# Performance work log

Measured on AMD Instinct MI355X. Metric: run time of the kernel, lower is better.

## Reference

```python
import jax, jax.numpy as jnp
import numpy as np

NUM_USERS = 100000
NUM_ITEMS = 50000
DIM_H = 64
NUM_LAYERS = 4
NUM_EDGES = 2000000


def setup_inputs() -> dict:
    key = jax.random.key(0)
    k1, k2, k3, k4 = jax.random.split(key, 4)
    emb_users = jax.random.normal(k1, (NUM_USERS, DIM_H), dtype=jnp.float32) * 0.01
    emb_items = jax.random.normal(k2, (NUM_ITEMS, DIM_H), dtype=jnp.float32) * 0.01
    edge_users = jax.random.randint(k3, (NUM_EDGES,), 0, NUM_USERS, dtype=jnp.int64)
    edge_items = jax.random.randint(k4, (NUM_EDGES,), 0, NUM_ITEMS, dtype=jnp.int64)
    edge_values = jnp.ones((NUM_EDGES,), dtype=jnp.float32)
    return {"emb_users": emb_users, "emb_items": emb_items,
            "edge_users": edge_users, "edge_items": edge_items,
            "edge_values": edge_values}


def reference(emb_users, emb_items, edge_users, edge_items, edge_values):
    U = emb_users.shape[0]
    I = emb_items.shape[0]
    N = U + I
    # Symmetric bipartite adjacency in COO form: (u, i+U) and (i+U, u).
    rows = jnp.concatenate([edge_users, edge_items + U])
    cols = jnp.concatenate([edge_items + U, edge_users])
    vals = jnp.concatenate([edge_values, edge_values])
    # D^{-1/2} A D^{-1/2} normalization (inf -> 0 for isolated nodes).
    deg = jax.ops.segment_sum(vals, rows, num_segments=N)
    dinv = jnp.where(deg > 0, jax.lax.rsqrt(jnp.maximum(deg, 1e-12)), 0.0)
    nvals = dinv[rows] * vals * dinv[cols]

    emb = jnp.concatenate([emb_users, emb_items])  # [N, d]
    acc = emb  # running sum over layer outputs (incl. layer 0)
    e = emb
    for _ in range(NUM_LAYERS):
        # SpMM: e <- A_norm @ e via gather + segment-sum scatter
        e = jax.ops.segment_sum(nvals[:, None] * e[cols], rows, num_segments=N)
        acc = acc + e
    alpha = 1.0 / (NUM_LAYERS + 1)
    # Original computes alpha * mean(stack(embs)), i.e. sum / (L+1)^2.
    emb_final = alpha * (acc / (NUM_LAYERS + 1))
    embf_users = emb_final[:U]
    embf_items = emb_final[U:]
    return (embf_users, emb_users, embf_items, emb_items)
```

## Files before the change

kernel.cpp:

```cpp
#include <hip/hip_runtime.h>


static inline size_t align_up(size_t x, size_t a) { return (x + a - 1) & ~(a - 1); }

#define BS_LOG 10
#define NBA 160
#define KB  1024
#define ENT 4096

__device__ inline unsigned short f32_to_bf16(float f) {
    unsigned int u = __float_as_uint(f);
    unsigned int r = (u + 0x7FFFu + ((u >> 16) & 1u)) >> 16;
    return (unsigned short)r;
}
__device__ inline float bf16_to_f32(unsigned short h) {
    return __uint_as_float(((unsigned int)h) << 16);
}
__device__ inline float bf16_lo(unsigned int d) {
    return __uint_as_float(d << 16);
}
__device__ inline float bf16_hi(unsigned int d) {
    return __uint_as_float(d & 0xFFFF0000u);
}

__global__ __launch_bounds__(256) void k_bucket_count(
        const int* __restrict__ eu, const int* __restrict__ ei,
        int* __restrict__ bh, int U, int E, int NB, int CH) {
    __shared__ int hist[NBA];
    int k = blockIdx.x;
    int t = threadIdx.x;
    if (t < NBA) hist[t] = 0;
    __syncthreads();
    int lo = k * CH, hi = min(E, lo + CH);
    for (int i = lo + t; i < hi; i += 256) {
        int u  = eu[i];
        int it = ei[i] + U;
        atomicAdd(&hist[u >> BS_LOG], 1);
        atomicAdd(&hist[it >> BS_LOG], 1);
    }
    __syncthreads();
    if (t < NB) bh[k * NBA + t] = hist[t];
}

__global__ __launch_bounds__(256) void k_scan_blocks(
        int* __restrict__ bh, int* __restrict__ total, int NB) {
    __shared__ int s[256];
    int b = blockIdx.x;
    int t = threadIdx.x;
    int k0 = t * 4;
    int vals[4];
    int sum = 0;
    #pragma unroll
    for (int j = 0; j < 4; ++j) { vals[j] = bh[(k0 + j) * NBA + b]; sum += vals[j]; }
    s[t] = sum;
    __syncthreads();
    for (int d = 1; d < 256; d <<= 1) {
        int v = (t >= d) ? s[t - d] : 0;
        __syncthreads();
        s[t] += v;
        __syncthreads();
    }
    int run = s[t] - sum;
    #pragma unroll
    for (int j = 0; j < 4; ++j) { int v = vals[j]; bh[(k0 + j) * NBA + b] = run; run += v; }
    if (t == 255) total[b] = run;
}

__global__ __launch_bounds__(256) void k_scan_buckets(
        const int* __restrict__ total, int* __restrict__ bbase, int NB) {
    __shared__ int s[256];
    int t = threadIdx.x;
    int v = (t < NB) ? (((total[t] + 3) & ~3) + 3072) : 0;
    s[t] = v;
    __syncthreads();
    for (int d = 1; d < 256; d <<= 1) {
        int x = (t >= d) ? s[t - d] : 0;
        __syncthreads();
        s[t] += x;
        __syncthreads();
    }
    if (t < NB) bbase[t] = s[t] - v;
}

__global__ __launch_bounds__(256) void k_bucket_scatter(
        const int* __restrict__ eu, const int* __restrict__ ei,
        const float* __restrict__ ev, const int* __restrict__ bh,
        int2* __restrict__ gb, int U, int E, int NB, int CH, int CAP) {
    __shared__ uint2 sent[ENT];
    __shared__ int   sdst[ENT];
    __shared__ int   lcur[NBA];
    __shared__ int   ldif[NBA];
    __shared__ int   sscan[256];
    __shared__ int   stot;
    int k = blockIdx.x;
    int t = threadIdx.x;
    if (t < NBA) lcur[t] = 0;
    __syncthreads();
    int lo = k * CH, hi = min(E, lo + CH);
    for (int i = lo + t; i < hi; i += 256) {
        int u  = eu[i];
        int it = ei[i] + U;
        atomicAdd(&lcur[u >> BS_LOG], 1);
        atomicAdd(&lcur[it >> BS_LOG], 1);
    }
    __syncthreads();
    int c = (t < NB) ? lcur[t] : 0;
    sscan[t] = c;
    __syncthreads();
    for (int d = 1; d < 256; d <<= 1) {
        int v = (t >= d) ? sscan[t - d] : 0;
        __syncthreads();
        sscan[t] += v;
        __syncthreads();
    }
    if (t < NB) {
        int st = sscan[t] - c;
        lcur[t] = st;
        ldif[t] = t * CAP + bh[k * NBA + t] - st;
    }
    if (t == 255) stot = sscan[255];
    __syncthreads();
    for (int i = lo + t; i < hi; i += 256) {
        int u  = eu[i];
        int it = ei[i] + U;
        unsigned vb = __float_as_uint(ev[i]);
        int b1 = u >> BS_LOG;
        int s1 = atomicAdd(&lcur[b1], 1);
        sent[s1] = make_uint2((unsigned)((u & 1023) | (it << 10)), vb);
        sdst[s1] = ldif[b1] + s1;
        int b2 = it >> BS_LOG;
        int s2 = atomicAdd(&lcur[b2], 1);
        sent[s2] = make_uint2((unsigned)((it & 1023) | (u << 10)), vb);
        sdst[s2] = ldif[b2] + s2;
    }
    __syncthreads();
    int tot = stot;
    for (int i = t; i < tot; i += 256) {
        uint2 e = sent[i];
        gb[sdst[i]] = make_int2((int)e.x, (int)e.y);
    }
}

__global__ __launch_bounds__(1024) void k_bucket_csr(
        const int2* __restrict__ gb, const int* __restrict__ total,
        const int* __restrict__ bbase,
        int* __restrict__ offs, int* __restrict__ cnt,
        float* __restrict__ dinv, float* __restrict__ dsq,
        int2* __restrict__ csr, int N, int CAP) {
    __shared__ int   hist[1024];
    __shared__ float degf[1024];
    __shared__ int   offl[1024];
    __shared__ int   scan[1024];
    int b = blockIdx.x;
    int t = threadIdx.x;
    int n0 = b << BS_LOG;
    int nbc = min(1024, N - n0);
    int cb = min(total[b], CAP);
    int base = bbase[b];
    const int2* gbb = gb + (size_t)b * CAP;

    hist[t] = 0;
    degf[t] = 0.f;
    __syncthreads();
    for (int i = t; i < cb; i += 1024) {
        int2 e = gbb[i];
        int rl = e.x & 1023;
        atomicAdd(&hist[rl], 1);
        atomicAdd(&degf[rl], __int_as_float(e.y));
    }
    __syncthreads();
    int h = hist[t];
    int h4 = (h + 3) & ~3;
    scan[t] = h4;
    __syncthreads();
    for (int d = 1; d < 1024; d <<= 1) {
        int v = (t >= d) ? scan[t - d] : 0;
        __syncthreads();
        scan[t] += v;
        __syncthreads();
    }
    int off4 = scan[t] - h4;
    offl[t] = off4;
    if (t < nbc) {
        int node = n0 + t;
        offs[node] = base + off4;
        cnt[node]  = h;
        float s = degf[t];
        bool pos = (s > 0.0f);
        dinv[node] = pos ? rsqrtf(fmaxf(s, 1e-12f)) : 0.0f;
        dsq[node]  = pos ? sqrtf(s) : 0.0f;
        for (int p = h; p < h4; ++p)
            csr[base + off4 + p] = make_int2(0, 0);
    }
    hist[t] = 0;
    __syncthreads();
    for (int i = t; i < cb; i += 1024) {
        int2 e = gbb[i];
        int rl = e.x & 1023;
        int col = (int)(((unsigned)e.x) >> 10);
        int tk = atomicAdd(&hist[rl], 1);
        csr[base + offl[rl] + tk] = make_int2(col, e.y);
    }
}

__global__ void k_init(const float4* __restrict__ emb_u, const float4* __restrict__ emb_i,
                       const float* __restrict__ dinv,
                       ushort4* __restrict__ g0, int U16, int N16) {
    int i = blockIdx.x * blockDim.x + threadIdx.x;
    if (i >= N16) return;
    float4 v = (i < U16) ? emb_u[i] : emb_i[i - U16];
    float d = dinv[i >> 4];
    ushort4 o;
    o.x = f32_to_bf16(v.x * d);
    o.y = f32_to_bf16(v.y * d);
    o.z = f32_to_bf16(v.z * d);
    o.w = f32_to_bf16(v.w * d);
    g0[i] = o;
}

__global__ __launch_bounds__(256) void k_layer(
        const uint4* __restrict__ gin, uint4* __restrict__ gout,
        const float* __restrict__ dinv,
        const int* __restrict__ offs, const int* __restrict__ cnt,
        const int2* __restrict__ csr, int N) {
    int gtid = blockIdx.x * blockDim.x + threadIdx.x;
    int row = gtid >> 3;
    unsigned q = threadIdx.x & 7;
    if (row >= N) return;
    int base = offs[row];
    int c = cnt[row];
    int nIter = (c + 3) >> 2;

    float a0 = 0.f, a1 = 0.f, a2 = 0.f, a3 = 0.f;
    float a4 = 0.f, a5 = 0.f, a6 = 0.f, a7 = 0.f;

    const uint4* ep4 = (const uint4*)(csr + base);
    uint4 E0 = make_uint4(0, 0, 0, 0), E1 = E0;
    if (nIter > 0) { E0 = ep4[0]; E1 = ep4[1]; }

    for (int i = 0; i < nIter; ++i) {
        uint4 G0 = gin[(E0.x << 3) | q];
        uint4 G1 = gin[(E0.z << 3) | q];
        uint4 G2 = gin[(E1.x << 3) | q];
        uint4 G3 = gin[(E1.z << 3) | q];
        uint4 P0 = ep4[2 * i + 2];
        uint4 P1 = ep4[2 * i + 3];
        float w0 = __uint_as_float(E0.y);
        float w1 = __uint_as_float(E0.w);
        float w2 = __uint_as_float(E1.y);
        float w3 = __uint_as_float(E1.w);
        a0 += w0 * bf16_lo(G0.x); a1 += w0 * bf16_hi(G0.x);
        a2 += w0 * bf16_lo(G0.y); a3 += w0 * bf16_hi(G0.y);
        a4 += w0 * bf16_lo(G0.z); a5 += w0 * bf16_hi(G0.z);
        a6 += w0 * bf16_lo(G0.w); a7 += w0 * bf16_hi(G0.w);
        a0 += w1 * bf16_lo(G1.x); a1 += w1 * bf16_hi(G1.x);
        a2 += w1 * bf16_lo(G1.y); a3 += w1 * bf16_hi(G1.y);
        a4 += w1 * bf16_lo(G1.z); a5 += w1 * bf16_hi(G1.z);
        a6 += w1 * bf16_lo(G1.w); a7 += w1 * bf16_hi(G1.w);
        a0 += w2 * bf16_lo(G2.x); a1 += w2 * bf16_hi(G2.x);
        a2 += w2 * bf16_lo(G2.y); a3 += w2 * bf16_hi(G2.y);
        a4 += w2 * bf16_lo(G2.z); a5 += w2 * bf16_hi(G2.z);
        a6 += w2 * bf16_lo(G2.w); a7 += w2 * bf16_hi(G2.w);
        a0 += w3 * bf16_lo(G3.x); a1 += w3 * bf16_hi(G3.x);
        a2 += w3 * bf16_lo(G3.y); a3 += w3 * bf16_hi(G3.y);
        a4 += w3 * bf16_lo(G3.z); a5 += w3 * bf16_hi(G3.z);
        a6 += w3 * bf16_lo(G3.w); a7 += w3 * bf16_hi(G3.w);
        E0 = P0; E1 = P1;
    }

    float dr = dinv[row];
    float d2 = dr * dr;
    uint4 o;
    o.x = (unsigned int)f32_to_bf16(d2 * a0) | ((unsigned int)f32_to_bf16(d2 * a1) << 16);
    o.y = (unsigned int)f32_to_bf16(d2 * a2) | ((unsigned int)f32_to_bf16(d2 * a3) << 16);
    o.z = (unsigned int)f32_to_bf16(d2 * a4) | ((unsigned int)f32_to_bf16(d2 * a5) << 16);
    o.w = (unsigned int)f32_to_bf16(d2 * a6) | ((unsigned int)f32_to_bf16(d2 * a7) << 16);
    gout[((unsigned)row << 3) | q] = o;
}

__global__ void k_final(const float4* __restrict__ emb_u, const float4* __restrict__ emb_i,
                        const ushort4* __restrict__ g1, const ushort4* __restrict__ g2,
                        const ushort4* __restrict__ g3, const ushort4* __restrict__ g4,
                        const float* __restrict__ dsq,
                        float4* __restrict__ out, int U16, int I16) {
    int i = blockIdx.x * blockDim.x + threadIdx.x;
    int total = 2 * U16 + 2 * I16;
    if (i >= total) return;
    const float s = 1.0f / 25.0f;
    float4 r;
    if (i < U16 || (i >= 2 * U16 && i < 2 * U16 + I16)) {
        int gi, node;
        float4 e0;
        if (i < U16) { gi = i; node = i >> 4; e0 = emb_u[i]; }
        else { int j = i - 2 * U16; gi = U16 + j; node = (U16 >> 4) + (j >> 4); e0 = emb_i[j]; }
        float d = dsq[node];
        ushort4 a = g1[gi], b = g2[gi], cc = g3[gi], dd = g4[gi];
        float gx = bf16_to_f32(a.x) + bf16_to_f32(b.x) + bf16_to_f32(cc.x) + bf16_to_f32(dd.x);
        float gy = bf16_to_f32(a.y) + bf16_to_f32(b.y) + bf16_to_f32(cc.y) + bf16_to_f32(dd.y);
        float gz = bf16_to_f32(a.z) + bf16_to_f32(b.z) + bf16_to_f32(cc.z) + bf16_to_f32(dd.z);
        float gw = bf16_to_f32(a.w) + bf16_to_f32(b.w) + bf16_to_f32(cc.w) + bf16_to_f32(dd.w);
        r = make_float4((e0.x + d * gx) * s, (e0.y + d * gy) * s,
                        (e0.z + d * gz) * s, (e0.w + d * gw) * s);
    } else if (i < 2 * U16) {
        r = emb_u[i - U16];
    } else {
        r = emb_i[i - 2 * U16 - I16];
    }
    out[i] = r;
}

extern "C" void kernel_launch(void* const* d_in, const int* in_sizes, int n_in,
                              void* d_out, int out_size, void* d_ws, size_t ws_size,
                              hipStream_t stream) {
    const float* emb_u = (const float*)d_in[0];
    const float* emb_i = (const float*)d_in[1];
    const int*   eu    = (const int*)d_in[2];
    const int*   ei    = (const int*)d_in[3];
    const float* ev    = (const float*)d_in[4];

    const int U = in_sizes[0] / 64;
    const int I = in_sizes[1] / 64;
    const int N = U + I;
    const int E = in_sizes[2];
    const int DE = 2 * E;

    const int NB = (N + 1023) >> BS_LOG;
    const int CH = (E + KB - 1) / KB;

    char* base = (char*)d_ws;
    size_t off = 0;
    int*   offs  = (int*)  (base + off); off = align_up(off + (size_t)N * 4, 256);
    int*   cnt   = (int*)  (base + off); off = align_up(off + (size_t)N * 4, 256);
    float* dinv  = (float*)(base + off); off = align_up(off + (size_t)N * 4, 256);
    float* dsq   = (float*)(base + off); off = align_up(off + (size_t)N * 4, 256);
    int*   bh    = (int*)  (base + off); off = align_up(off + (size_t)NBA * KB * 4, 256);
    int*   total = (int*)  (base + off); off = align_up(off + (size_t)NBA * 4, 256);
    int*   bbase = (int*)  (base + off); off = align_up(off + (size_t)NBA * 4, 256);
    int2*  csr   = (int2*) (base + off);
    off = align_up(off + ((size_t)DE + (size_t)NBA * 3080 + 32) * 8, 256);
    unsigned short* g[5];
    for (int l = 0; l < 5; ++l) {
        g[l] = (unsigned short*)(base + off);
        off = align_up(off + (size_t)N * 64 * 2, 256);
    }
    (void)ws_size;

    int2* gb = (int2*)g[1];
    size_t gcap = (size_t)4 * N * 128;
    int CAP = (int)(gcap / ((size_t)NB * 8));
    if (CAP > 65536) CAP = 65536;

    const int B = 256;
    k_bucket_count  <<<KB, B, 0, stream>>>(eu, ei, bh, U, E, NB, CH);
    k_scan_blocks   <<<NB, B, 0, stream>>>(bh, total, NB);
    k_scan_buckets  <<<1,  B, 0, stream>>>(total, bbase, NB);
    k_bucket_scatter<<<KB, B, 0, stream>>>(eu, ei, ev, bh, gb, U, E, NB, CH, CAP);
    k_bucket_csr    <<<NB, 1024, 0, stream>>>(gb, total, bbase, offs, cnt, dinv, dsq, csr, N, CAP);

    const int U16 = U * 16, I16 = I * 16, N16 = N * 16;
    k_init<<<(N16 + B - 1) / B, B, 0, stream>>>((const float4*)emb_u, (const float4*)emb_i,
                                                dinv, (ushort4*)g[0], U16, N16);

    for (int layer = 0; layer < 4; ++layer) {
        int threads = N * 8;
        k_layer<<<(threads + B - 1) / B, B, 0, stream>>>(
            (const uint4*)g[layer], (uint4*)g[layer + 1], dinv, offs, cnt, csr, N);
    }

    int totalv4 = 2 * U16 + 2 * I16;
    k_final<<<(totalv4 + B - 1) / B, B, 0, stream>>>(
        (const float4*)emb_u, (const float4*)emb_i,
        (const ushort4*)g[1], (const ushort4*)g[2], (const ushort4*)g[3], (const ushort4*)g[4],
        dsq, (float4*)d_out, U16, I16);
}
```

Baseline: 543.0 us.

## Split per-bucket CSR build into sub-bucket count, scan, and place kernels

Replaces the single 1024-thread-per-bucket CSR construction kernel with three stages: a 256-thread count kernel per quarter-bucket that computes degrees and local offsets, a global scan over sub-bucket sizes, and a placement kernel per quarter-bucket. The aim is more blocks in flight (4x) and tighter CSR packing with less padding, which removes the per-bucket 3072 slack. In exchange, each sub-block rereads the whole bucket and filters by sub-range, so bucket edge reads go up fourfold, and there is one extra launch.

Measured after the change: 589.0 us. +8.5%, slower.

```diff
diff --git a/kernel.cpp b/kernel.cpp
--- a/kernel.cpp
+++ b/kernel.cpp
@@ -64,22 +64,6 @@
     #pragma unroll
     for (int j = 0; j < 4; ++j) { int v = vals[j]; bh[(k0 + j) * NBA + b] = run; run += v; }
     if (t == 255) total[b] = run;
-}
-
-__global__ __launch_bounds__(256) void k_scan_buckets(
-        const int* __restrict__ total, int* __restrict__ bbase, int NB) {
-    __shared__ int s[256];
-    int t = threadIdx.x;
-    int v = (t < NB) ? (((total[t] + 3) & ~3) + 3072) : 0;
-    s[t] = v;
-    __syncthreads();
-    for (int d = 1; d < 256; d <<= 1) {
-        int x = (t >= d) ? s[t - d] : 0;
-        __syncthreads();
-        s[t] += x;
-        __syncthreads();
-    }
-    if (t < NB) bbase[t] = s[t] - v;
 }
 
 __global__ __launch_bounds__(256) void k_bucket_scatter(
@@ -141,65 +125,103 @@
     }
 }
 
-__global__ __launch_bounds__(1024) void k_bucket_csr(
+__global__ __launch_bounds__(256) void k_node_count(
         const int2* __restrict__ gb, const int* __restrict__ total,
-        const int* __restrict__ bbase,
-        int* __restrict__ offs, int* __restrict__ cnt,
-        float* __restrict__ dinv, float* __restrict__ dsq,
-        int2* __restrict__ csr, int N, int CAP) {
-    __shared__ int   hist[1024];
-    __shared__ float degf[1024];
-    __shared__ int   offl[1024];
-    __shared__ int   scan[1024];
-    int b = blockIdx.x;
-    int t = threadIdx.x;
-    int n0 = b << BS_LOG;
-    int nbc = min(1024, N - n0);
+        int* __restrict__ cnt, float* __restrict__ dinv, float* __restrict__ dsq,
+        int* __restrict__ loffs, int* __restrict__ ssum,
+        int N, int CAP) {
+    __shared__ int   hist[256];
+    __shared__ float degf[256];
+    __shared__ int   scan[256];
+    int s = blockIdx.x;
+    int b = s >> 2, sub = s & 3;
+    int t = threadIdx.x;
     int cb = min(total[b], CAP);
-    int base = bbase[b];
     const int2* gbb = gb + (size_t)b * CAP;
-
     hist[t] = 0;
     degf[t] = 0.f;
     __syncthreads();
-    for (int i = t; i < cb; i += 1024) {
+    for (int i = t; i < cb; i += 256) {
         int2 e = gbb[i];
         int rl = e.x & 1023;
-        atomicAdd(&hist[rl], 1);
-        atomicAdd(&degf[rl], __int_as_float(e.y));
+        if ((rl >> 8) == sub) {
+            atomicAdd(&hist[rl & 255], 1);
+            atomicAdd(&degf[rl & 255], __int_as_float(e.y));
+        }
     }
     __syncthreads();
     int h = hist[t];
     int h4 = (h + 3) & ~3;
     scan[t] = h4;
     __syncthreads();
+    for (int d = 1; d < 256; d <<= 1) {
+        int v = (t >= d) ? scan[t - d] : 0;
+        __syncthreads();
+        scan[t] += v;
+        __syncthreads();
+    }
+    int node = (b << BS_LOG) + (sub << 8) + t;
+    if (node < N) {
+        cnt[node]   = h;
+        loffs[node] = scan[t] - h4;
+        float sd = degf[t];
+        bool pos = (sd > 0.0f);
+        dinv[node] = pos ? rsqrtf(fmaxf(sd, 1e-12f)) : 0.0f;
+        dsq[node]  = pos ? sqrtf(sd) : 0.0f;
+    }
+    if (t == 255) ssum[s] = scan[255];
+}
+
+__global__ __launch_bounds__(1024) void k_scan_sub(
+        const int* __restrict__ ssum, int* __restrict__ sbase, int NS) {
+    __shared__ int s[1024];
+    int t = threadIdx.x;
+    int v = (t < NS) ? ssum[t] : 0;
+    s[t] = v;
+    __syncthreads();
     for (int d = 1; d < 1024; d <<= 1) {
-        int v = (t >= d) ? scan[t - d] : 0;
-        __syncthreads();
-        scan[t] += v;
-        __syncthreads();
-    }
-    int off4 = scan[t] - h4;
-    offl[t] = off4;
-    if (t < nbc) {
-        int node = n0 + t;
-        offs[node] = base + off4;
-        cnt[node]  = h;
-        float s = degf[t];
-        bool pos = (s > 0.0f);
-        dinv[node] = pos ? rsqrtf(fmaxf(s, 1e-12f)) : 0.0f;
-        dsq[node]  = pos ? sqrtf(s) : 0.0f;
+        int x = (t >= d) ? s[t - d] : 0;
+        __syncthreads();
+        s[t] += x;
+        __syncthreads();
+    }
+    if (t < NS) sbase[t] = s[t] - v;
+}
+
+__global__ __launch_bounds__(256) void k_csr_place(
+        const int2* __restrict__ gb, const int* __restrict__ total,
+        const int* __restrict__ sbase, const int* __restrict__ cnt,
+        const int* __restrict__ loffs,
+        int* __restrict__ offs, int2* __restrict__ csr, int N, int CAP) {
+    __shared__ int lofs[256];
+    __shared__ int cur[256];
+    int s = blockIdx.x;
+    int b = s >> 2, sub = s & 3;
+    int t = threadIdx.x;
+    int cb = min(total[b], CAP);
+    int base = sbase[s];
+    const int2* gbb = gb + (size_t)b * CAP;
+    int node = (b << BS_LOG) + (sub << 8) + t;
+    int lo = 0, h = 0;
+    if (node < N) { lo = loffs[node]; h = cnt[node]; }
+    lofs[t] = lo;
+    cur[t] = 0;
+    if (node < N) {
+        offs[node] = base + lo;
+        int h4 = (h + 3) & ~3;
         for (int p = h; p < h4; ++p)
-            csr[base + off4 + p] = make_int2(0, 0);
-    }
-    hist[t] = 0;
-    __syncthreads();
-    for (int i = t; i < cb; i += 1024) {
+            csr[base + lo + p] = make_int2(0, 0);
+    }
+    __syncthreads();
+    for (int i = t; i < cb; i += 256) {
         int2 e = gbb[i];
         int rl = e.x & 1023;
-        int col = (int)(((unsigned)e.x) >> 10);
-        int tk = atomicAdd(&hist[rl], 1);
-        csr[base + offl[rl] + tk] = make_int2(col, e.y);
+        if ((rl >> 8) == sub) {
+            int r = rl & 255;
+            int tk = atomicAdd(&cur[r], 1);
+            int col = (int)(((unsigned)e.x) >> 10);
+            csr[base + lofs[r] + tk] = make_int2(col, e.y);
+        }
     }
 }
 
@@ -325,6 +347,7 @@
     const int DE = 2 * E;
 
     const int NB = (N + 1023) >> BS_LOG;
+    const int NS = NB * 4;
     const int CH = (E + KB - 1) / KB;
 
     char* base = (char*)d_ws;
@@ -333,11 +356,13 @@
     int*   cnt   = (int*)  (base + off); off = align_up(off + (size_t)N * 4, 256);
     float* dinv  = (float*)(base + off); off = align_up(off + (size_t)N * 4, 256);
     float* dsq   = (float*)(base + off); off = align_up(off + (size_t)N * 4, 256);
+    int*   loffs = (int*)  (base + off); off = align_up(off + (size_t)N * 4, 256);
     int*   bh    = (int*)  (base + off); off = align_up(off + (size_t)NBA * KB * 4, 256);
     int*   total = (int*)  (base + off); off = align_up(off + (size_t)NBA * 4, 256);
-    int*   bbase = (int*)  (base + off); off = align_up(off + (size_t)NBA * 4, 256);
+    int*   ssum  = (int*)  (base + off); off = align_up(off + (size_t)NBA * 4 * 4, 256);
+    int*   sbase = (int*)  (base + off); off = align_up(off + (size_t)NBA * 4 * 4, 256);
     int2*  csr   = (int2*) (base + off);
-    off = align_up(off + ((size_t)DE + (size_t)NBA * 3080 + 32) * 8, 256);
+    off = align_up(off + ((size_t)DE + (size_t)N * 4 + 64) * 8, 256);
     unsigned short* g[5];
     for (int l = 0; l < 5; ++l) {
         g[l] = (unsigned short*)(base + off);
@@ -353,9 +378,10 @@
     const int B = 256;
     k_bucket_count  <<<KB, B, 0, stream>>>(eu, ei, bh, U, E, NB, CH);
     k_scan_blocks   <<<NB, B, 0, stream>>>(bh, total, NB);
-    k_scan_buckets  <<<1,  B, 0, stream>>>(total, bbase, NB);
     k_bucket_scatter<<<KB, B, 0, stream>>>(eu, ei, ev, bh, gb, U, E, NB, CH, CAP);
-    k_bucket_csr    <<<NB, 1024, 0, stream>>>(gb, total, bbase, offs, cnt, dinv, dsq, csr, N, CAP);
+    k_node_count    <<<NS, B, 0, stream>>>(gb, total, cnt, dinv, dsq, loffs, ssum, N, CAP);
+    k_scan_sub      <<<1, 1024, 0, stream>>>(ssum, sbase, NS);
+    k_csr_place     <<<NS, B, 0, stream>>>(gb, total, sbase, cnt, loffs, offs, csr, N, CAP);
 
     const int U16 = U * 16, I16 = I * 16, N16 = N * 16;
     k_init<<<(N16 + B - 1) / B, B, 0, stream>>>((const float4*)emb_u, (const float4*)emb_i,
```
